# Performance work log

Hardware: AMD Instinct MI355X
Metric: run time of the kernel (lower is better)

The kernel has to match this reference:

```python
import jax, jax.numpy as jnp
import numpy as np

# Model constants (from init_kwargs)
N_ATOMS = 30000
N_PAIRS = 300000
NF_IN = 64
NF_OUT = 64
N_DIST = 20
MIND_SOFT = 0.85
MAXD_SOFT = 5.0
HARD_CUTOFF = 6.5


def setup_inputs() -> dict:
    key = jax.random.key(0)
    k = jax.random.split(key, 8)
    in_features = jax.random.normal(k[0], (N_ATOMS, NF_IN), dtype=jnp.float32)
    pair_first = jax.random.randint(k[1], (N_PAIRS,), 0, N_ATOMS)
    pair_second = jax.random.randint(k[2], (N_PAIRS,), 0, N_ATOMS)
    dist_pairs = jax.random.uniform(k[3], (N_PAIRS,), dtype=jnp.float32,
                                    minval=MIND_SOFT, maxval=HARD_CUTOFF)
    # InverseSensitivityModule init: mu uniformly spaced in inverse-distance space
    mu = jnp.linspace(1.0 / MAXD_SOFT, 1.0 / MIND_SOFT, N_DIST, dtype=jnp.float32)
    sigma = jnp.full((N_DIST,), (1.0 / MIND_SOFT - 1.0 / MAXD_SOFT) / N_DIST,
                     dtype=jnp.float32)
    # xavier-normal-ish init scales
    int_weights = jax.random.normal(k[4], (N_DIST, NF_OUT, NF_IN), dtype=jnp.float32) \
        * np.sqrt(2.0 / (NF_IN + NF_OUT)).astype(np.float32)
    w_self = jax.random.normal(k[5], (NF_OUT, NF_IN), dtype=jnp.float32) \
        * np.sqrt(2.0 / (NF_IN + NF_OUT)).astype(np.float32)
    b_self = jax.random.normal(k[6], (NF_OUT,), dtype=jnp.float32) * 0.01
    return {"in_features": in_features, "pair_first": pair_first,
            "pair_second": pair_second, "dist_pairs": dist_pairs,
            "mu": mu, "sigma": sigma, "int_weights": int_weights,
            "w_self": w_self, "b_self": b_self}


def _sensitivity(dist, mu, sigma):
    # Inverse-distance Gaussian sensitivities with smooth cosine hard cutoff.
    inv_d = 1.0 / dist  # [P]
    gauss = jnp.exp(-0.5 * ((inv_d[:, None] - mu[None, :]) / sigma[None, :]) ** 2)  # [P, n_dist]
    cut = jnp.cos(0.5 * jnp.pi * dist / HARD_CUTOFF) ** 2
    cut = jnp.where(dist < HARD_CUTOFF, cut, 0.0)
    return gauss * cut[:, None]


def reference(in_features, pair_first, pair_second, dist_pairs,
              mu, sigma, int_weights, w_self, b_self):
    n_atoms = in_features.shape[0]
    sense = _sensitivity(dist_pairs, mu, sigma)              # [P, n_dist]
    # envsum: env[a, nu, f] = sum_{p: pair_first[p]==a} sense[p, nu] * in_features[pair_second[p], f]
    neigh = in_features[pair_second]                          # [P, nf_in] gather
    contrib = sense[:, :, None] * neigh[:, None, :]           # [P, n_dist, nf_in]
    env = jax.ops.segment_sum(
        contrib.reshape(contrib.shape[0], N_DIST * NF_IN),
        pair_first, num_segments=n_atoms)                     # [A, n_dist*nf_in]
    # interaction matmul: weights permuted (n_dist, nf_in, nf_out) then flattened
    weights_rs = jnp.transpose(int_weights, (0, 2, 1)).reshape(N_DIST * NF_IN, NF_OUT)
    features_out = env @ weights_rs                           # [A, nf_out]
    features_out += in_features @ w_self.T + b_self           # self interaction
    return features_out
```

## Files before the change

### kernel.cpp

```cpp
#include <hip/hip_runtime.h>
#include <math.h>

#define N_ATOMS    30000
#define N_PAIRS    300000
#define CAP        48
#define NF         64
#define ND         20
#define K_ENV      1280
#define K_TOT      1344
#define NKSTEP     42
#define KSH        21
#define HARD_CUT   6.5f
#define BA         16
#define ESTRIDE    1352
#define NM1        ((unsigned)(N_ATOMS - 1))

#define INVD_LO    0.15384615385f
#define INVD_RANGE 1.02262443439f
#define QS         (65535.0f / INVD_RANGE)
#define DQ         (INVD_RANGE / 65535.0f)
#define NEXP2      (-0.7213475204444817f)

typedef short    s16x8  __attribute__((ext_vector_type(8)));
typedef __bf16   bf16x8 __attribute__((ext_vector_type(8)));
typedef unsigned u32x4  __attribute__((ext_vector_type(4)));
typedef float    f32x4  __attribute__((ext_vector_type(4)));
typedef float    f32x16 __attribute__((ext_vector_type(16)));

typedef __attribute__((address_space(1))) const void gconst_void;
typedef __attribute__((address_space(3))) void       lds_void;

__device__ __forceinline__ unsigned short f2bf(float x) {
    union { float f; unsigned u; } v; v.f = x;
    unsigned r = v.u + 0x7fffu + ((v.u >> 16) & 1u);
    return (unsigned short)(r >> 16);
}
__device__ __forceinline__ unsigned pkbf(float a, float b) {
    return (unsigned)f2bf(a) | ((unsigned)f2bf(b) << 16);
}
__device__ __forceinline__ unsigned pkbf2(float a, float b) {
    unsigned au = __float_as_uint(a) + 0x8000u;
    unsigned bu = __float_as_uint(b) + 0x8000u;
    return __builtin_amdgcn_perm(bu, au, 0x07060302u);
}
__device__ __forceinline__ float senseval(unsigned w0, unsigned lcb,
                                          float zA, float zB) {
    float uu = (float)(w0 & 0xffffu);
    float z  = __builtin_fmaf(uu, zA, zB);
    float ar = __builtin_fmaf(z * z, NEXP2, __uint_as_float(lcb));
    return __builtin_amdgcn_exp2f(ar);
}

__global__ void k_prep(const float* __restrict__ iw, const float* __restrict__ wself,
                       const float* __restrict__ mu, const float* __restrict__ sigma,
                       const float* __restrict__ x,
                       unsigned short* __restrict__ WtB, int* __restrict__ cnts,
                       float2* __restrict__ msr, unsigned* __restrict__ xb16) {
    if (blockIdx.x < 42) {
        int idx = blockIdx.x * 256 + threadIdx.x;
        if (idx >= NKSTEP * 4 * 64) return;
        int l  = idx & 63;
        int q  = (idx >> 6) & 3;
        int ks = idx >> 8;
        int n  = q * 16 + (l & 15);
        int kb = ks * 32 + (l >> 4) * 8;
        u32x4 u;
        #pragma unroll
        for (int jj = 0; jj < 4; jj++) {
            unsigned short lo, hi;
            #pragma unroll
            for (int e = 0; e < 2; e++) {
                int k = kb + 2 * jj + e;
                float val;
                if (k < K_ENV) {
                    int t  = k / 640;
                    int rm = k - t * 640;
                    int g  = rm >> 7;
                    int c  = (rm & 127) >> 2;
                    int r  = k & 3;
                    int nu = 4 * g + r;
                    int f  = 2 * c + t;
                    val = iw[(nu * NF + n) * NF + f];
                } else {
                    val = wself[n * NF + (k - K_ENV)];
                }
                if (e == 0) lo = f2bf(val); else hi = f2bf(val);
            }
            u[jj] = (unsigned)lo | ((unsigned)hi << 16);
        }
        *(u32x4*)&WtB[idx * 8] = u;
    } else if (blockIdx.x < 160) {
        int i = (blockIdx.x - 42) * 256 + threadIdx.x;
        if (i < N_ATOMS) cnts[i] = 0;
    } else if (blockIdx.x == 160) {
        int i = threadIdx.x;
        if (i < ND) { float2 m; m.x = mu[i]; m.y = 1.0f / sigma[i]; msr[i] = m; }
    } else {
        int o = (blockIdx.x - 161) * 256 + threadIdx.x;
        if (o < N_ATOMS * 32 / 4) {
            int wbase = o * 4;
            const float* src = &x[(size_t)wbase * 2];
            float2 f0 = *(const float2*)(src);
            float2 f1 = *(const float2*)(src + 2);
            float2 f2 = *(const float2*)(src + 4);
            float2 f3 = *(const float2*)(src + 6);
            u32x4 u;
            u[0] = pkbf(f0.x, f0.y);
            u[1] = pkbf(f1.x, f1.y);
            u[2] = pkbf(f2.x, f2.y);
            u[3] = pkbf(f3.x, f3.y);
            *(u32x4*)&xb16[wbase] = u;
        }
    }
}

__global__ void k_scatter(const int* __restrict__ first, const int* __restrict__ second,
                          const float* __restrict__ dist, int* __restrict__ cnts,
                          uint2* __restrict__ pk) {
    int p = (blockIdx.x * 256 + threadIdx.x) * 2;
    if (p >= N_PAIRS) return;
    int2   f2 = *(const int2*)&first[p];
    int2   s2 = *(const int2*)&second[p];
    float2 d2 = *(const float2*)&dist[p];
    {
        float d    = d2.x;
        float invd = 1.0f / d;
        float tq   = fmaxf((invd - INVD_LO) * QS + 0.5f, 0.0f);
        unsigned u = min((unsigned)tq, 65535u);
        float co   = __cosf(0.2416609733530613f * d);
        float lc   = fmaxf(__log2f(co * co), -10000.0f);
        int pos = atomicAdd(&cnts[f2.x], 1);
        if (pos < CAP) {
            uint2 v; v.x = ((unsigned)s2.x << 16) | u; v.y = __float_as_uint(lc);
            pk[(size_t)f2.x * CAP + pos] = v;
        }
    }
    {
        float d    = d2.y;
        float invd = 1.0f / d;
        float tq   = fmaxf((invd - INVD_LO) * QS + 0.5f, 0.0f);
        unsigned u = min((unsigned)tq, 65535u);
        float co   = __cosf(0.2416609733530613f * d);
        float lc   = fmaxf(__log2f(co * co), -10000.0f);
        int pos = atomicAdd(&cnts[f2.y], 1);
        if (pos < CAP) {
            uint2 v; v.x = ((unsigned)s2.y << 16) | u; v.y = __float_as_uint(lc);
            pk[(size_t)f2.y * CAP + pos] = v;
        }
    }
}

__global__ void __launch_bounds__(512, 6)
k_main(const unsigned* __restrict__ xb16, const int* __restrict__ cnts,
       const uint2* __restrict__ pk, const float2* __restrict__ msr,
       const unsigned short* __restrict__ WtB, const float* __restrict__ bself,
       float* __restrict__ out) {
    __shared__ unsigned short env[BA * ESTRIDE];
    __shared__ uint2 pkl[BA * CAP];
    const int t  = threadIdx.x;
    const int w  = t >> 6;
    const int l  = t & 63;
    const int h  = l >> 5;
    const int cl = l & 31;
    const int a0 = blockIdx.x * BA;

    if (w < 6) {
        const char* gsrc = (const char*)(pk + (size_t)a0 * CAP) + (w * 64 + l) * 16;
        char* ldst = (char*)pkl + w * 1024;
        __builtin_amdgcn_global_load_lds((gconst_void*)gsrc, (lds_void*)ldst, 16, 0, 0);
    }

    float2 ms   = msr[min(cl, ND - 1)];
    const bool  nuok = (cl < ND);
    const float isig = ms.y;
    const float zA   = nuok ? DQ * isig : 0.0f;
    const float zB   = nuok ? (INVD_LO * isig - ms.x * isig) : 1.0e19f;
    const unsigned* xw = xb16 + cl;

    const int cntA = min(cnts[a0 + 2 * w + 0], CAP);
    const int cntB = min(cnts[a0 + 2 * w + 1], CAP);

    __syncthreads();

    {
        uint2 pz; pz.x = 0u; pz.y = 0xFF800000u;
        if (l < CAP) {
            if (l >= cntA) pkl[(2 * w + 0) * CAP + l] = pz;
            if (l >= cntB) pkl[(2 * w + 1) * CAP + l] = pz;
        }
    }

    #pragma unroll 1
    for (int ci = 0; ci < 2; ci++) {
        const int i = 2 * w + ci;
        const int a = a0 + i;
        const int cnt = ci ? cntB : cntA;
        const int nst = max((cnt + 15) >> 4, 1);
        const uint2* gb = &pkl[i * CAP];
        f32x16 acc0 = {0.f}, acc1 = {0.f};
        #pragma unroll 1
        for (int ks = 0; ks < nst; ks++) {
            const int k0 = ks * 16 + h * 8;
            const uint2* bp = gb + k0;
            uint4 q0 = *(const uint4*)(bp + 0);
            uint4 q1 = *(const uint4*)(bp + 2);
            uint4 q2 = *(const uint4*)(bp + 4);
            uint4 q3 = *(const uint4*)(bp + 6);
            unsigned g0 = xw[(q0.x >> 16) * 32];
            unsigned g1 = xw[(q0.z >> 16) * 32];
            unsigned g2 = xw[(q1.x >> 16) * 32];
            unsigned g3 = xw[(q1.z >> 16) * 32];
            unsigned g4 = xw[(q2.x >> 16) * 32];
            unsigned g5 = xw[(q2.z >> 16) * 32];
            unsigned g6 = xw[(q3.x >> 16) * 32];
            unsigned g7 = xw[(q3.z >> 16) * 32];
            u32x4 A, B0, B1;
            A[0] = pkbf2(senseval(q0.x, q0.y, zA, zB),
                         senseval(q0.z, q0.w, zA, zB));
            A[1] = pkbf2(senseval(q1.x, q1.y, zA, zB),
                         senseval(q1.z, q1.w, zA, zB));
            A[2] = pkbf2(senseval(q2.x, q2.y, zA, zB),
                         senseval(q2.z, q2.w, zA, zB));
            A[3] = pkbf2(senseval(q3.x, q3.y, zA, zB),
                         senseval(q3.z, q3.w, zA, zB));
            B0[0] = __builtin_amdgcn_perm(g1, g0, 0x05040100u);
            B0[1] = __builtin_amdgcn_perm(g3, g2, 0x05040100u);
            B0[2] = __builtin_amdgcn_perm(g5, g4, 0x05040100u);
            B0[3] = __builtin_amdgcn_perm(g7, g6, 0x05040100u);
            B1[0] = __builtin_amdgcn_perm(g1, g0, 0x07060302u);
            B1[1] = __builtin_amdgcn_perm(g3, g2, 0x07060302u);
            B1[2] = __builtin_amdgcn_perm(g5, g4, 0x07060302u);
            B1[3] = __builtin_amdgcn_perm(g7, g6, 0x07060302u);
            acc0 = __builtin_amdgcn_mfma_f32_32x32x16_bf16(
                       __builtin_bit_cast(bf16x8, A),
                       __builtin_bit_cast(bf16x8, B0), acc0, 0, 0, 0);
            acc1 = __builtin_amdgcn_mfma_f32_32x32x16_bf16(
                       __builtin_bit_cast(bf16x8, A),
                       __builtin_bit_cast(bf16x8, B1), acc1, 0, 0, 0);
        }
        unsigned short* er = &env[i * ESTRIDE];
        #pragma unroll
        for (int q = 0; q < 3; q++) {
            int g = 2 * q + h;
            if (g < 5) {
                uint2 v0, v1;
                v0.x = pkbf2(acc0[4 * q + 0], acc0[4 * q + 1]);
                v0.y = pkbf2(acc0[4 * q + 2], acc0[4 * q + 3]);
                v1.x = pkbf2(acc1[4 * q + 0], acc1[4 * q + 1]);
                v1.y = pkbf2(acc1[4 * q + 2], acc1[4 * q + 3]);
                *(uint2*)&er[g * 128 + cl * 4]       = v0;
                *(uint2*)&er[640 + g * 128 + cl * 4] = v1;
            }
        }
        unsigned sw = xb16[(size_t)a * 32 + (l >> 1)];
        er[K_ENV + l] = (unsigned short)(sw >> ((l & 1) * 16));
    }

    const int wq     = w & 3;
    const int ksbase = (w >> 2) * KSH;
    const unsigned short* wb = &WtB[((ksbase * 4 + wq) * 64 + l) * 8];
    s16x8 b0 = *(const s16x8*)(wb);
    s16x8 b1 = *(const s16x8*)(wb + 2048);
    s16x8 b2 = *(const s16x8*)(wb + 4096);
    s16x8 b3 = *(const s16x8*)(wb + 6144);
    float bs = (w < 4) ? bself[wq * 16 + (l & 15)] : 0.f;
    __syncthreads();

    {
        const int m16  = l & 15;
        const int quad = l >> 4;
        f32x4 acc = {0.f, 0.f, 0.f, 0.f};
        for (int kk = 0; kk < KSH; kk++) {
            int ks = ksbase + kk;
            s16x8 afrag = *(const s16x8*)&env[m16 * ESTRIDE + ks * 32 + quad * 8];
            s16x8 bcur = b0;
            b0 = b1; b1 = b2; b2 = b3;
            int nx = (kk + 4 < KSH) ? kk + 4 : KSH - 1;
            b3 = *(const s16x8*)(wb + (size_t)nx * 2048);
            acc = __builtin_amdgcn_mfma_f32_16x16x32_bf16(
                      __builtin_bit_cast(bf16x8, afrag),
                      __builtin_bit_cast(bf16x8, bcur), acc, 0, 0, 0);
        }
        float* red = (float*)pkl;
        if (w >= 4) {
            *(f32x4*)&red[((w - 4) * 64 + l) * 4] = acc;
        }
        __syncthreads();
        if (w < 4) {
            f32x4 other = *(const f32x4*)&red[(w * 64 + l) * 4];
            #pragma unroll
            for (int r = 0; r < 4; r++) {
                int row = quad * 4 + r;
                out[(size_t)(a0 + row) * NF + wq * 16 + m16] = acc[r] + other[r] + bs;
            }
        }
    }
}

extern "C" void kernel_launch(void* const* d_in, const int* in_sizes, int n_in,
                              void* d_out, int out_size, void* d_ws, size_t ws_size,
                              hipStream_t stream) {
    const float* x      = (const float*)d_in[0];
    const int*   first  = (const int*)d_in[1];
    const int*   second = (const int*)d_in[2];
    const float* dist   = (const float*)d_in[3];
    const float* mu     = (const float*)d_in[4];
    const float* sigma  = (const float*)d_in[5];
    const float* iw     = (const float*)d_in[6];
    const float* wself  = (const float*)d_in[7];
    const float* bself  = (const float*)d_in[8];
    float* out = (float*)d_out;

    char* ws = (char*)d_ws;
    unsigned short* WtB  = (unsigned short*)(ws);
    int*            cnts = (int*)(ws + 172032);
    float2*         msr  = (float2*)(ws + 292032);
    uint2*          pk   = (uint2*)(ws + 292192);
    unsigned*       xb16 = (unsigned*)(ws + 11812192);

    k_prep<<<dim3(161 + (N_ATOMS * 8 + 255) / 256), dim3(256), 0, stream>>>(
        iw, wself, mu, sigma, x, WtB, cnts, msr, xb16);
    k_scatter<<<dim3((N_PAIRS / 2 + 255) / 256), dim3(256), 0, stream>>>(
        first, second, dist, cnts, pk);
    k_main<<<dim3(N_ATOMS / BA), dim3(512), 0, stream>>>(
        xb16, cnts, pk, msr, WtB, bself, out);
}
```

Before: 117.2 us.

## Fuse prep and scatter kernels, memset counters, trim sense and bf16 pack math

Measured after the change: 116.4 us. Within noise of the previous version (-0.6%).

```diff
diff --git a/kernel.cpp b/kernel.cpp
--- a/kernel.cpp
+++ b/kernel.cpp
@@ -19,7 +19,7 @@
 #define INVD_RANGE 1.02262443439f
 #define QS         (65535.0f / INVD_RANGE)
 #define DQ         (INVD_RANGE / 65535.0f)
-#define NEXP2      (-0.7213475204444817f)
+#define SQC        0.8493218002880191f
 
 typedef short    s16x8  __attribute__((ext_vector_type(8)));
 typedef __bf16   bf16x8 __attribute__((ext_vector_type(8)));
@@ -43,19 +43,27 @@
     unsigned bu = __float_as_uint(b) + 0x8000u;
     return __builtin_amdgcn_perm(bu, au, 0x07060302u);
 }
+__device__ __forceinline__ unsigned cvtpk(float a, float b) {
+    unsigned r;
+    asm("v_cvt_pk_bf16_f32 %0, %1, %2" : "=v"(r) : "v"(a), "v"(b));
+    return r;
+}
 __device__ __forceinline__ float senseval(unsigned w0, unsigned lcb,
                                           float zA, float zB) {
     float uu = (float)(w0 & 0xffffu);
-    float z  = __builtin_fmaf(uu, zA, zB);
-    float ar = __builtin_fmaf(z * z, NEXP2, __uint_as_float(lcb));
+    float zz = __builtin_fmaf(uu, zA, zB);
+    float ar = __builtin_fmaf(zz, -zz, __uint_as_float(lcb));
     return __builtin_amdgcn_exp2f(ar);
 }
 
-__global__ void k_prep(const float* __restrict__ iw, const float* __restrict__ wself,
-                       const float* __restrict__ mu, const float* __restrict__ sigma,
-                       const float* __restrict__ x,
-                       unsigned short* __restrict__ WtB, int* __restrict__ cnts,
-                       float2* __restrict__ msr, unsigned* __restrict__ xb16) {
+__global__ void k_ps(const float* __restrict__ iw, const float* __restrict__ wself,
+                     const float* __restrict__ mu, const float* __restrict__ sigma,
+                     const float* __restrict__ x,
+                     const int* __restrict__ first, const int* __restrict__ second,
+                     const float* __restrict__ dist,
+                     unsigned short* __restrict__ WtB, int* __restrict__ cnts,
+                     float2* __restrict__ msr, unsigned* __restrict__ xb16,
+                     uint2* __restrict__ pk) {
     if (blockIdx.x < 42) {
         int idx = blockIdx.x * 256 + threadIdx.x;
         if (idx >= NKSTEP * 4 * 64) return;
@@ -89,14 +97,11 @@
             u[jj] = (unsigned)lo | ((unsigned)hi << 16);
         }
         *(u32x4*)&WtB[idx * 8] = u;
-    } else if (blockIdx.x < 160) {
-        int i = (blockIdx.x - 42) * 256 + threadIdx.x;
-        if (i < N_ATOMS) cnts[i] = 0;
-    } else if (blockIdx.x == 160) {
+    } else if (blockIdx.x == 42) {
         int i = threadIdx.x;
         if (i < ND) { float2 m; m.x = mu[i]; m.y = 1.0f / sigma[i]; msr[i] = m; }
-    } else {
-        int o = (blockIdx.x - 161) * 256 + threadIdx.x;
+    } else if (blockIdx.x < 981) {
+        int o = (blockIdx.x - 43) * 256 + threadIdx.x;
         if (o < N_ATOMS * 32 / 4) {
             int wbase = o * 4;
             const float* src = &x[(size_t)wbase * 2];
@@ -111,41 +116,37 @@
             u[3] = pkbf(f3.x, f3.y);
             *(u32x4*)&xb16[wbase] = u;
         }
-    }
-}
-
-__global__ void k_scatter(const int* __restrict__ first, const int* __restrict__ second,
-                          const float* __restrict__ dist, int* __restrict__ cnts,
-                          uint2* __restrict__ pk) {
-    int p = (blockIdx.x * 256 + threadIdx.x) * 2;
-    if (p >= N_PAIRS) return;
-    int2   f2 = *(const int2*)&first[p];
-    int2   s2 = *(const int2*)&second[p];
-    float2 d2 = *(const float2*)&dist[p];
-    {
-        float d    = d2.x;
-        float invd = 1.0f / d;
-        float tq   = fmaxf((invd - INVD_LO) * QS + 0.5f, 0.0f);
-        unsigned u = min((unsigned)tq, 65535u);
-        float co   = __cosf(0.2416609733530613f * d);
-        float lc   = fmaxf(__log2f(co * co), -10000.0f);
-        int pos = atomicAdd(&cnts[f2.x], 1);
-        if (pos < CAP) {
-            uint2 v; v.x = ((unsigned)s2.x << 16) | u; v.y = __float_as_uint(lc);
-            pk[(size_t)f2.x * CAP + pos] = v;
-        }
-    }
-    {
-        float d    = d2.y;
-        float invd = 1.0f / d;
-        float tq   = fmaxf((invd - INVD_LO) * QS + 0.5f, 0.0f);
-        unsigned u = min((unsigned)tq, 65535u);
-        float co   = __cosf(0.2416609733530613f * d);
-        float lc   = fmaxf(__log2f(co * co), -10000.0f);
-        int pos = atomicAdd(&cnts[f2.y], 1);
-        if (pos < CAP) {
-            uint2 v; v.x = ((unsigned)s2.y << 16) | u; v.y = __float_as_uint(lc);
-            pk[(size_t)f2.y * CAP + pos] = v;
+    } else {
+        int p = ((blockIdx.x - 981) * 256 + threadIdx.x) * 2;
+        if (p >= N_PAIRS) return;
+        int2   f2 = *(const int2*)&first[p];
+        int2   s2 = *(const int2*)&second[p];
+        float2 d2 = *(const float2*)&dist[p];
+        {
+            float d    = d2.x;
+            float invd = 1.0f / d;
+            float tq   = fmaxf((invd - INVD_LO) * QS + 0.5f, 0.0f);
+            unsigned u = min((unsigned)tq, 65535u);
+            float co   = __cosf(0.2416609733530613f * d);
+            float lc   = fmaxf(__log2f(co * co), -10000.0f);
+            int pos = atomicAdd(&cnts[f2.x], 1);
+            if (pos < CAP) {
+                uint2 v; v.x = ((unsigned)s2.x << 16) | u; v.y = __float_as_uint(lc);
+                pk[(size_t)f2.x * CAP + pos] = v;
+            }
+        }
+        {
+            float d    = d2.y;
+            float invd = 1.0f / d;
+            float tq   = fmaxf((invd - INVD_LO) * QS + 0.5f, 0.0f);
+            unsigned u = min((unsigned)tq, 65535u);
+            float co   = __cosf(0.2416609733530613f * d);
+            float lc   = fmaxf(__log2f(co * co), -10000.0f);
+            int pos = atomicAdd(&cnts[f2.y], 1);
+            if (pos < CAP) {
+                uint2 v; v.x = ((unsigned)s2.y << 16) | u; v.y = __float_as_uint(lc);
+                pk[(size_t)f2.y * CAP + pos] = v;
+            }
         }
     }
 }
@@ -173,8 +174,8 @@
     float2 ms   = msr[min(cl, ND - 1)];
     const bool  nuok = (cl < ND);
     const float isig = ms.y;
-    const float zA   = nuok ? DQ * isig : 0.0f;
-    const float zB   = nuok ? (INVD_LO * isig - ms.x * isig) : 1.0e19f;
+    const float zA   = nuok ? DQ * isig * SQC : 0.0f;
+    const float zB   = nuok ? ((INVD_LO - ms.x) * isig * SQC) : 8.493e18f;
     const unsigned* xw = xb16 + cl;
 
     const int cntA = min(cnts[a0 + 2 * w + 0], CAP);
@@ -244,10 +245,10 @@
             int g = 2 * q + h;
             if (g < 5) {
                 uint2 v0, v1;
-                v0.x = pkbf2(acc0[4 * q + 0], acc0[4 * q + 1]);
-                v0.y = pkbf2(acc0[4 * q + 2], acc0[4 * q + 3]);
-                v1.x = pkbf2(acc1[4 * q + 0], acc1[4 * q + 1]);
-                v1.y = pkbf2(acc1[4 * q + 2], acc1[4 * q + 3]);
+                v0.x = cvtpk(acc0[4 * q + 0], acc0[4 * q + 1]);
+                v0.y = cvtpk(acc0[4 * q + 2], acc0[4 * q + 3]);
+                v1.x = cvtpk(acc1[4 * q + 0], acc1[4 * q + 1]);
+                v1.y = cvtpk(acc1[4 * q + 2], acc1[4 * q + 3]);
                 *(uint2*)&er[g * 128 + cl * 4]       = v0;
                 *(uint2*)&er[640 + g * 128 + cl * 4] = v1;
             }
@@ -318,10 +319,9 @@
     uint2*          pk   = (uint2*)(ws + 292192);
     unsigned*       xb16 = (unsigned*)(ws + 11812192);
 
-    k_prep<<<dim3(161 + (N_ATOMS * 8 + 255) / 256), dim3(256), 0, stream>>>(
-        iw, wself, mu, sigma, x, WtB, cnts, msr, xb16);
-    k_scatter<<<dim3((N_PAIRS / 2 + 255) / 256), dim3(256), 0, stream>>>(
-        first, second, dist, cnts, pk);
+    hipMemsetAsync(cnts, 0, N_ATOMS * sizeof(int), stream);
+    k_ps<<<dim3(981 + (N_PAIRS / 2 + 255) / 256), dim3(256), 0, stream>>>(
+        iw, wself, mu, sigma, x, first, second, dist, WtB, cnts, msr, xb16, pk);
     k_main<<<dim3(N_ATOMS / BA), dim3(512), 0, stream>>>(
         xb16, cnts, pk, msr, WtB, bself, out);
 }
```
